# Kernel tuning notes

Hardware: AMD Instinct MI355X
Metric: run time of the kernel (lower is better)

## Reference

```python
import jax, jax.numpy as jnp
import numpy as np

B, T, C = 32, 2048, 1024  # batch, seq_len (<= block_size), n_embd
HEAD_SIZE = 128


def setup_inputs() -> dict:
    key = jax.random.key(0)
    kx, kk, kq, kv = jax.random.split(key, 4)
    std = 0.02  # CustomLinear init: normal(0, 0.02)
    return {
        "x": jax.random.normal(kx, (B, T, C), dtype=jnp.float32),
        "Wk": jax.random.normal(kk, (HEAD_SIZE, C), dtype=jnp.float32) * std,
        "Wq": jax.random.normal(kq, (HEAD_SIZE, C), dtype=jnp.float32) * std,
        "Wv": jax.random.normal(kv, (HEAD_SIZE, C), dtype=jnp.float32) * std,
    }


def reference(x, Wk, Wq, Wv):
    # x: [B, T, C]; W*: [head_size, C] (torch Linear layout, no bias)
    Bb, Tt, Cc = x.shape
    k = jnp.einsum("btc,hc->bth", x, Wk)
    q = jnp.einsum("btc,hc->bth", x, Wq)
    v = jnp.einsum("btc,hc->bth", x, Wv)
    # NOTE: original scales by C**-0.5 (n_embd), not head_size**-0.5
    wei = jnp.einsum("bth,bsh->bts", q, k) * (Cc ** -0.5)
    causal = jnp.tril(jnp.ones((Tt, Tt), dtype=bool))  # tril[:T,:T]
    wei = jnp.where(causal, wei, -jnp.inf)
    wei = jax.nn.softmax(wei, axis=-1)
    return jnp.einsum("bts,bsh->bth", wei, v)  # [B, T, head_size]
```

## Files before the change

### kernel.cpp

```cpp
#include <hip/hip_runtime.h>
#include <hip/hip_bf16.h>

typedef __bf16 bf8_t __attribute__((ext_vector_type(8)));
typedef __bf16 bf4_t __attribute__((ext_vector_type(4)));
typedef float f4_t __attribute__((ext_vector_type(4)));

#define B_ 32
#define T_ 2048
#define C_ 1024
#define H_ 128

__global__ __launch_bounds__(256) void wconv_kernel(
    const float* __restrict__ Wk, const float* __restrict__ Wq, const float* __restrict__ Wv,
    __bf16* __restrict__ Wr)
{
    const int e  = (blockIdx.x * 256 + threadIdx.x) * 8;
    const int kk = e & 31;
    const int lr = (e >> 5) & 15;
    const int ks = (e >> 9) & 31;
    const int cg = e >> 14;
    const int col = cg * 16 + lr;
    const int k   = ks * 32 + kk;
    const float* W = (col < 128) ? Wk : (col < 256) ? Wq : Wv;
    const float* p = W + (size_t)(col & 127) * C_ + k;
    float4 f0 = *(const float4*)p;
    float4 f1 = *(const float4*)(p + 4);
    bf8_t o;
    o[0] = (__bf16)f0.x; o[1] = (__bf16)f0.y; o[2] = (__bf16)f0.z; o[3] = (__bf16)f0.w;
    o[4] = (__bf16)f1.x; o[5] = (__bf16)f1.y; o[6] = (__bf16)f1.z; o[7] = (__bf16)f1.w;
    *(bf8_t*)(Wr + e) = o;
}

__global__ __launch_bounds__(256) void proj_kernel(
    const float* __restrict__ x, const __bf16* __restrict__ Wr,
    __bf16* __restrict__ Kb, __bf16* __restrict__ Qb, __bf16* __restrict__ VtG)
{
    __shared__ __bf16 As[128 * 64];
    __shared__ __bf16 Bs[2][16 * 512];

    const int bid  = blockIdx.x;
    const int xcd  = bid & 7;
    const int slot = bid >> 3;
    const int nt   = slot % 3;
    const int m0   = ((slot / 3) * 8 + xcd) * 128;
    const int tid  = threadIdx.x;
    const int lane = tid & 63;
    const int w    = tid >> 6;
    const int wqm  = w >> 1;
    const int wqn  = w & 1;
    const int lr   = lane & 15;
    const int quad = lane >> 4;

    f4_t acc[4][4];
    #pragma unroll
    for (int mi = 0; mi < 4; mi++)
        #pragma unroll
        for (int ni = 0; ni < 4; ni++) acc[mi][ni] = f4_t{0.f, 0.f, 0.f, 0.f};

    float4 pf[8];

#define LOADA(t) { _Pragma("unroll") \
    for (int i_ = 0; i_ < 8; ++i_) { \
        const int u_ = i_ * 256 + tid; \
        pf[i_] = *(const float4*)(x + (size_t)(m0 + (u_ >> 4)) * C_ + (t) * 64 + (u_ & 15) * 4); } }

#define WRITEA { _Pragma("unroll") \
    for (int i_ = 0; i_ < 8; ++i_) { \
        const int u_ = i_ * 256 + tid; \
        const int r_ = u_ >> 4; \
        float4 f_ = pf[i_]; \
        *(bf4_t*)&As[r_ * 64 + ((((u_ & 15) * 4)) ^ ((r_ & 7) * 8))] = \
            bf4_t{(__bf16)f_.x, (__bf16)f_.y, (__bf16)f_.z, (__bf16)f_.w}; } }

#define STAGEB(t, bsel) { _Pragma("unroll") \
    for (int i_ = 0; i_ < 4; ++i_) { \
        const int ci_ = i_ * 4 + w; \
        const __bf16* src_ = Wr + ((size_t)((nt * 8 + (ci_ >> 1)) * 32 + (t) * 2 + (ci_ & 1)) << 9) + lane * 8; \
        __builtin_amdgcn_global_load_lds( \
            (const __attribute__((address_space(1))) void*)src_, \
            (__attribute__((address_space(3))) void*)&Bs[bsel][ci_ << 9], 16, 0, 0); } }

    LOADA(0)
    STAGEB(0, 0)
    WRITEA
    __syncthreads();

    #pragma unroll 2
    for (int t = 0; t < 16; ++t) {
        const int bsel = t & 1;
        if (t < 15) {
            LOADA(t + 1)
            STAGEB(t + 1, bsel ^ 1)
        }
        #pragma unroll
        for (int kh = 0; kh < 2; ++kh) {
            bf8_t af[4], bfr[4];
            #pragma unroll
            for (int mi = 0; mi < 4; ++mi) {
                const int row = wqm * 64 + mi * 16 + lr;
                af[mi] = *(const bf8_t*)&As[row * 64 + ((kh * 32 + quad * 8) ^ ((row & 7) * 8))];
            }
            #pragma unroll
            for (int ni = 0; ni < 4; ++ni) {
                const int ch = (wqn * 4 + ni) * 2 + kh;
                bfr[ni] = *(const bf8_t*)&Bs[bsel][ch * 512 + lr * 32 + quad * 8];
            }
            if (nt < 2) {
                #pragma unroll
                for (int mi = 0; mi < 4; ++mi)
                    #pragma unroll
                    for (int ni = 0; ni < 4; ++ni)
                        acc[mi][ni] = __builtin_amdgcn_mfma_f32_16x16x32_bf16(af[mi], bfr[ni], acc[mi][ni], 0, 0, 0);
            } else {
                #pragma unroll
                for (int mi = 0; mi < 4; ++mi)
                    #pragma unroll
                    for (int ni = 0; ni < 4; ++ni)
                        acc[mi][ni] = __builtin_amdgcn_mfma_f32_16x16x32_bf16(bfr[ni], af[mi], acc[mi][ni], 0, 0, 0);
            }
        }
        __syncthreads();
        if (t < 15) {
            WRITEA
            __syncthreads();
        }
    }

#undef LOADA
#undef WRITEA
#undef STAGEB

    if (nt < 2) {
        __bf16* Out = nt ? Qb : Kb;
        #pragma unroll
        for (int ni = 0; ni < 4; ++ni)
            #pragma unroll
            for (int mi = 0; mi < 4; ++mi) {
                const int col = wqn * 64 + ni * 16 + lr;
                #pragma unroll
                for (int r = 0; r < 4; ++r) {
                    const int row = m0 + wqm * 64 + mi * 16 + quad * 4 + r;
                    Out[(size_t)row * H_ + col] = (__bf16)acc[mi][ni][r];
                }
            }
    } else {
        const int bb = m0 >> 11;
        const int t0 = m0 & (T_ - 1);
        #pragma unroll
        for (int ni = 0; ni < 4; ++ni)
            #pragma unroll
            for (int mi = 0; mi < 4; ++mi) {
                const int tok = t0 + wqm * 64 + mi * 16 + lr;
                #pragma unroll
                for (int r = 0; r < 4; ++r) {
                    const int h = wqn * 64 + ni * 16 + quad * 4 + r;
                    VtG[(size_t)bb * H_ * T_ + (size_t)h * T_ + tok] = (__bf16)acc[mi][ni][r];
                }
            }
    }
}

__global__ __launch_bounds__(256, 2) void flash_kernel(
    const __bf16* __restrict__ Qb, const __bf16* __restrict__ Kb,
    const __bf16* __restrict__ VtG, float* __restrict__ Out)
{
    __shared__ __bf16 Ks[64][136];
    __shared__ __bf16 Vt[128][72];
    __shared__ __bf16 Ps[128][72];

    const int qt = (blockIdx.y < 16) ? (15 - blockIdx.x) : blockIdx.x;
    const int b  = blockIdx.y;
    const size_t kqbase = (size_t)b * T_ * H_;
    const size_t vbase  = (size_t)b * H_ * T_;

    const int tid  = threadIdx.x;
    const int lane = tid & 63;
    const int w    = tid >> 6;
    const int lr   = lane & 15;
    const int quad = lane >> 4;

    bf8_t qf[2][4];
    #pragma unroll
    for (int m = 0; m < 2; m++) {
        const __bf16* qp = Qb + kqbase + (size_t)(qt * 128 + w * 32 + m * 16 + lr) * H_ + quad * 8;
        #pragma unroll
        for (int ks = 0; ks < 4; ks++) qf[m][ks] = *(const bf8_t*)(qp + ks * 32);
    }

    f4_t o[2][8];
    #pragma unroll
    for (int m = 0; m < 2; m++)
        #pragma unroll
        for (int n = 0; n < 8; n++) o[m][n] = f4_t{0.f, 0.f, 0.f, 0.f};
    float ls[2] = {0.f, 0.f};

    const float sc = 0.03125f * 1.4426950408889634f;
    const int jmax = 2 * qt + 1;

    int kR[4], kC[4], vH[4], vS[4];
    #pragma unroll
    for (int i = 0; i < 4; i++) {
        const int u = tid + i * 256;
        kR[i] = u >> 4;  kC[i] = (u & 15) << 3;
        vH[i] = u >> 3;  vS[i] = (u & 7) << 3;
    }
    bf8_t kr[4], vr[4];
    #pragma unroll
    for (int i = 0; i < 4; i++) {
        kr[i] = *(const bf8_t*)(Kb + kqbase + (size_t)kR[i] * H_ + kC[i]);
        vr[i] = *(const bf8_t*)(VtG + vbase + (size_t)vH[i] * T_ + vS[i]);
    }

    for (int j = 0; j <= jmax; j++) {
        __syncthreads();
        #pragma unroll
        for (int i = 0; i < 4; i++) {
            *(bf8_t*)&Ks[kR[i]][kC[i]] = kr[i];
            *(bf8_t*)&Vt[vH[i]][vS[i]] = vr[i];
        }
        __syncthreads();
        if (j < jmax) {
            const int s0 = (j + 1) * 64;
            #pragma unroll
            for (int i = 0; i < 4; i++) {
                kr[i] = *(const bf8_t*)(Kb + kqbase + (size_t)(s0 + kR[i]) * H_ + kC[i]);
                vr[i] = *(const bf8_t*)(VtG + vbase + (size_t)vH[i] * T_ + s0 + vS[i]);
            }
        }
        if (j == jmax && w < 2) continue;

        f4_t s4[2][4];
        #pragma unroll
        for (int m = 0; m < 2; m++)
            #pragma unroll
            for (int n = 0; n < 4; n++) s4[m][n] = f4_t{0.f, 0.f, 0.f, 0.f};
        #pragma unroll
        for (int ks = 0; ks < 4; ks++)
            #pragma unroll
            for (int n = 0; n < 4; n++) {
                bf8_t kf = *(const bf8_t*)&Ks[n * 16 + lr][ks * 32 + quad * 8];
                s4[0][n] = __builtin_amdgcn_mfma_f32_16x16x32_bf16(kf, qf[0][ks], s4[0][n], 0, 0, 0);
                s4[1][n] = __builtin_amdgcn_mfma_f32_16x16x32_bf16(kf, qf[1][ks], s4[1][n], 0, 0, 0);
            }

        const bool domask = (j == 2 * qt + (w >> 1));
        const int jrel = (j - 2 * qt) * 64;
        #pragma unroll
        for (int m = 0; m < 2; m++) {
            const int qg = w * 32 + m * 16 + lr;
            #pragma unroll
            for (int n = 0; n < 4; n++) {
                bf4_t pk;
                #pragma unroll
                for (int r = 0; r < 4; r++) {
                    float p = __builtin_exp2f(s4[m][n][r] * sc);
                    const int kg = jrel + n * 16 + quad * 4 + r;
                    if (domask && kg > qg) p = 0.f;
                    ls[m] += p;
                    pk[r] = (__bf16)p;
                }
                *(bf4_t*)&Ps[w * 32 + m * 16 + lr][n * 16 + quad * 4] = pk;
            }
        }

        #pragma unroll
        for (int ks = 0; ks < 2; ks++) {
            bf8_t pf0 = *(const bf8_t*)&Ps[w * 32 + lr][ks * 32 + quad * 8];
            bf8_t pf1 = *(const bf8_t*)&Ps[w * 32 + 16 + lr][ks * 32 + quad * 8];
            #pragma unroll
            for (int n = 0; n < 8; n++) {
                bf8_t vf = *(const bf8_t*)&Vt[n * 16 + lr][ks * 32 + quad * 8];
                o[0][n] = __builtin_amdgcn_mfma_f32_16x16x32_bf16(pf0, vf, o[0][n], 0, 0, 0);
                o[1][n] = __builtin_amdgcn_mfma_f32_16x16x32_bf16(pf1, vf, o[1][n], 0, 0, 0);
            }
        }
    }

    float inv[2][4];
    #pragma unroll
    for (int m = 0; m < 2; m++) {
        float v = ls[m];
        v += __shfl_xor(v, 16);
        v += __shfl_xor(v, 32);
        const float iv = 1.f / v;
        #pragma unroll
        for (int r = 0; r < 4; r++)
            inv[m][r] = __shfl(iv, quad * 4 + r);
    }
    #pragma unroll
    for (int m = 0; m < 2; m++)
        #pragma unroll
        for (int n = 0; n < 8; n++) {
            const int col = n * 16 + lr;
            #pragma unroll
            for (int r = 0; r < 4; r++) {
                const int row = qt * 128 + w * 32 + m * 16 + quad * 4 + r;
                Out[kqbase + (size_t)row * H_ + col] = o[m][n][r] * inv[m][r];
            }
        }
}

extern "C" void kernel_launch(void* const* d_in, const int* in_sizes, int n_in,
                              void* d_out, int out_size, void* d_ws, size_t ws_size,
                              hipStream_t stream) {
    const float* x  = (const float*)d_in[0];
    const float* Wk = (const float*)d_in[1];
    const float* Wq = (const float*)d_in[2];
    const float* Wv = (const float*)d_in[3];
    float* out = (float*)d_out;

    const size_t n_kqv = (size_t)B_ * T_ * H_;
    __bf16* Kb  = (__bf16*)d_ws;
    __bf16* Qb  = Kb + n_kqv;
    __bf16* VtG = Qb + n_kqv;
    __bf16* Wr  = VtG + n_kqv;

    wconv_kernel<<<dim3(192), 256, 0, stream>>>(Wk, Wq, Wv, Wr);
    proj_kernel<<<dim3(512 * 3), 256, 0, stream>>>(x, Wr, Kb, Qb, VtG);
    flash_kernel<<<dim3(16, B_), 256, 0, stream>>>(Qb, Kb, VtG, out);
}
```

Baseline: 472.9 us.

## Pair causal 64-row query tiles per block for balanced flash attention work

The flash kernel now processes 64-row query tiles instead of 128-row ones. Each block handles two tiles, qp and 31-qp, one after the other, so every block does about the same number of causal KV iterations. Each wave now owns 16 query rows instead of 32. This lowers register use and LDS size for the P buffer and removes the wave-idle skip on the diagonal block. The trade-off is that each K/V tile loaded into LDS now feeds half as much MFMA work, so total K/V traffic roughly doubles. The prefetch on the last iteration also issues a redundant load of tile 0.

```diff
diff --git a/kernel.cpp b/kernel.cpp
--- a/kernel.cpp
+++ b/kernel.cpp
@@ -166,10 +166,10 @@
 {
     __shared__ __bf16 Ks[64][136];
     __shared__ __bf16 Vt[128][72];
-    __shared__ __bf16 Ps[128][72];
-
-    const int qt = (blockIdx.y < 16) ? (15 - blockIdx.x) : blockIdx.x;
-    const int b  = blockIdx.y;
+    __shared__ __bf16 Ps[64][72];
+
+    const int b  = blockIdx.x;
+    const int qp = blockIdx.y;
     const size_t kqbase = (size_t)b * T_ * H_;
     const size_t vbase  = (size_t)b * H_ * T_;
 
@@ -179,23 +179,7 @@
     const int lr   = lane & 15;
     const int quad = lane >> 4;
 
-    bf8_t qf[2][4];
-    #pragma unroll
-    for (int m = 0; m < 2; m++) {
-        const __bf16* qp = Qb + kqbase + (size_t)(qt * 128 + w * 32 + m * 16 + lr) * H_ + quad * 8;
-        #pragma unroll
-        for (int ks = 0; ks < 4; ks++) qf[m][ks] = *(const bf8_t*)(qp + ks * 32);
-    }
-
-    f4_t o[2][8];
-    #pragma unroll
-    for (int m = 0; m < 2; m++)
-        #pragma unroll
-        for (int n = 0; n < 8; n++) o[m][n] = f4_t{0.f, 0.f, 0.f, 0.f};
-    float ls[2] = {0.f, 0.f};
-
     const float sc = 0.03125f * 1.4426950408889634f;
-    const int jmax = 2 * qt + 1;
 
     int kR[4], kC[4], vH[4], vS[4];
     #pragma unroll
@@ -204,6 +188,7 @@
         kR[i] = u >> 4;  kC[i] = (u & 15) << 3;
         vH[i] = u >> 3;  vS[i] = (u & 7) << 3;
     }
+
     bf8_t kr[4], vr[4];
     #pragma unroll
     for (int i = 0; i < 4; i++) {
@@ -211,93 +196,94 @@
         vr[i] = *(const bf8_t*)(VtG + vbase + (size_t)vH[i] * T_ + vS[i]);
     }
 
-    for (int j = 0; j <= jmax; j++) {
-        __syncthreads();
-        #pragma unroll
-        for (int i = 0; i < 4; i++) {
-            *(bf8_t*)&Ks[kR[i]][kC[i]] = kr[i];
-            *(bf8_t*)&Vt[vH[i]][vS[i]] = vr[i];
-        }
-        __syncthreads();
-        if (j < jmax) {
-            const int s0 = (j + 1) * 64;
+    for (int seg = 0; seg < 2; ++seg) {
+        const int qt   = seg ? (31 - qp) : qp;
+        const int jmax = qt;
+
+        bf8_t qf[4];
+        {
+            const __bf16* qpr = Qb + kqbase + (size_t)(qt * 64 + w * 16 + lr) * H_ + quad * 8;
+            #pragma unroll
+            for (int ks = 0; ks < 4; ks++) qf[ks] = *(const bf8_t*)(qpr + ks * 32);
+        }
+
+        f4_t o[8];
+        #pragma unroll
+        for (int n = 0; n < 8; n++) o[n] = f4_t{0.f, 0.f, 0.f, 0.f};
+        float ls = 0.f;
+
+        for (int j = 0; j <= jmax; ++j) {
+            __syncthreads();
             #pragma unroll
             for (int i = 0; i < 4; i++) {
-                kr[i] = *(const bf8_t*)(Kb + kqbase + (size_t)(s0 + kR[i]) * H_ + kC[i]);
-                vr[i] = *(const bf8_t*)(VtG + vbase + (size_t)vH[i] * T_ + s0 + vS[i]);
-            }
-        }
-        if (j == jmax && w < 2) continue;
-
-        f4_t s4[2][4];
-        #pragma unroll
-        for (int m = 0; m < 2; m++)
-            #pragma unroll
-            for (int n = 0; n < 4; n++) s4[m][n] = f4_t{0.f, 0.f, 0.f, 0.f};
-        #pragma unroll
-        for (int ks = 0; ks < 4; ks++)
-            #pragma unroll
-            for (int n = 0; n < 4; n++) {
-                bf8_t kf = *(const bf8_t*)&Ks[n * 16 + lr][ks * 32 + quad * 8];
-                s4[0][n] = __builtin_amdgcn_mfma_f32_16x16x32_bf16(kf, qf[0][ks], s4[0][n], 0, 0, 0);
-                s4[1][n] = __builtin_amdgcn_mfma_f32_16x16x32_bf16(kf, qf[1][ks], s4[1][n], 0, 0, 0);
-            }
-
-        const bool domask = (j == 2 * qt + (w >> 1));
-        const int jrel = (j - 2 * qt) * 64;
-        #pragma unroll
-        for (int m = 0; m < 2; m++) {
-            const int qg = w * 32 + m * 16 + lr;
+                *(bf8_t*)&Ks[kR[i]][kC[i]] = kr[i];
+                *(bf8_t*)&Vt[vH[i]][vS[i]] = vr[i];
+            }
+            __syncthreads();
+            {
+                const int s0 = (j < jmax) ? (j + 1) * 64 : 0;
+                #pragma unroll
+                for (int i = 0; i < 4; i++) {
+                    kr[i] = *(const bf8_t*)(Kb + kqbase + (size_t)(s0 + kR[i]) * H_ + kC[i]);
+                    vr[i] = *(const bf8_t*)(VtG + vbase + (size_t)vH[i] * T_ + s0 + vS[i]);
+                }
+            }
+
+            f4_t s4[4];
+            #pragma unroll
+            for (int n = 0; n < 4; n++) s4[n] = f4_t{0.f, 0.f, 0.f, 0.f};
+            #pragma unroll
+            for (int ks = 0; ks < 4; ks++)
+                #pragma unroll
+                for (int n = 0; n < 4; n++) {
+                    bf8_t kf = *(const bf8_t*)&Ks[n * 16 + lr][ks * 32 + quad * 8];
+                    s4[n] = __builtin_amdgcn_mfma_f32_16x16x32_bf16(kf, qf[ks], s4[n], 0, 0, 0);
+                }
+
+            const bool dm = (j == jmax);
+            const int qg = w * 16 + lr;
             #pragma unroll
             for (int n = 0; n < 4; n++) {
                 bf4_t pk;
                 #pragma unroll
                 for (int r = 0; r < 4; r++) {
-                    float p = __builtin_exp2f(s4[m][n][r] * sc);
-                    const int kg = jrel + n * 16 + quad * 4 + r;
-                    if (domask && kg > qg) p = 0.f;
-                    ls[m] += p;
+                    float p = __builtin_exp2f(s4[n][r] * sc);
+                    if (dm && (n * 16 + quad * 4 + r) > qg) p = 0.f;
+                    ls += p;
                     pk[r] = (__bf16)p;
                 }
-                *(bf4_t*)&Ps[w * 32 + m * 16 + lr][n * 16 + quad * 4] = pk;
-            }
-        }
-
-        #pragma unroll
-        for (int ks = 0; ks < 2; ks++) {
-            bf8_t pf0 = *(const bf8_t*)&Ps[w * 32 + lr][ks * 32 + quad * 8];
-            bf8_t pf1 = *(const bf8_t*)&Ps[w * 32 + 16 + lr][ks * 32 + quad * 8];
-            #pragma unroll
-            for (int n = 0; n < 8; n++) {
-                bf8_t vf = *(const bf8_t*)&Vt[n * 16 + lr][ks * 32 + quad * 8];
-                o[0][n] = __builtin_amdgcn_mfma_f32_16x16x32_bf16(pf0, vf, o[0][n], 0, 0, 0);
-                o[1][n] = __builtin_amdgcn_mfma_f32_16x16x32_bf16(pf1, vf, o[1][n], 0, 0, 0);
-            }
-        }
-    }
-
-    float inv[2][4];
-    #pragma unroll
-    for (int m = 0; m < 2; m++) {
-        float v = ls[m];
+                *(bf4_t*)&Ps[w * 16 + lr][n * 16 + quad * 4] = pk;
+            }
+
+            #pragma unroll
+            for (int ks = 0; ks < 2; ks++) {
+                bf8_t pfr = *(const bf8_t*)&Ps[w * 16 + lr][ks * 32 + quad * 8];
+                #pragma unroll
+                for (int n = 0; n < 8; n++) {
+                    bf8_t vf = *(const bf8_t*)&Vt[n * 16 + lr][ks * 32 + quad * 8];
+                    o[n] = __builtin_amdgcn_mfma_f32_16x16x32_bf16(pfr, vf, o[n], 0, 0, 0);
+                }
+            }
+        }
+
+        float v = ls;
         v += __shfl_xor(v, 16);
         v += __shfl_xor(v, 32);
         const float iv = 1.f / v;
-        #pragma unroll
-        for (int r = 0; r < 4; r++)
-            inv[m][r] = __shfl(iv, quad * 4 + r);
-    }
-    #pragma unroll
-    for (int m = 0; m < 2; m++)
+        float inv[4];
+        #pragma unroll
+        for (int r = 0; r < 4; r++) inv[r] = __shfl(iv, quad * 4 + r);
+
         #pragma unroll
         for (int n = 0; n < 8; n++) {
             const int col = n * 16 + lr;
             #pragma unroll
             for (int r = 0; r < 4; r++) {
-                const int row = qt * 128 + w * 32 + m * 16 + quad * 4 + r;
-                Out[kqbase + (size_t)row * H_ + col] = o[m][n][r] * inv[m][r];
-            }
-        }
+                const int row = qt * 64 + w * 16 + quad * 4 + r;
+                Out[kqbase + (size_t)row * H_ + col] = o[n][r] * inv[r];
+            }
+        }
+    }
 }
 
 extern "C" void kernel_launch(void* const* d_in, const int* in_sizes, int n_in,
@@ -317,5 +303,5 @@
 
     wconv_kernel<<<dim3(192), 256, 0, stream>>>(Wk, Wq, Wv, Wr);
     proj_kernel<<<dim3(512 * 3), 256, 0, stream>>>(x, Wr, Kb, Qb, VtG);
-    flash_kernel<<<dim3(16, B_), 256, 0, stream>>>(Qb, Kb, VtG, out);
+    flash_kernel<<<dim3(32, 16), 256, 0, stream>>>(Qb, Kb, VtG, out);
 }
```

Result: no change. 470.5 us (-0.5%).
